# Optimization experiments

Hardware: AMD Instinct MI355X
Metric: run time of the kernel (lower is better)

The kernel has to match this reference:

```python
import jax, jax.numpy as jnp
import numpy as np

B, T, IN, CELL, OUT = 512, 32, 512, 128, 128


def setup_inputs() -> dict:
    key = jax.random.key(0)
    ks = jax.random.split(key, 6)
    d = IN + CELL
    w = lambda k, shape, fan: jax.random.normal(k, shape, jnp.float32) / np.sqrt(fan).astype(np.float32)
    return {
        "x": jax.random.normal(ks[0], (B, T, IN), jnp.float32),
        "Wf": w(ks[1], (d, CELL), d), "bf": jnp.zeros((CELL,), jnp.float32),
        "Wi1": w(ks[2], (d, CELL), d), "bi1": jnp.zeros((CELL,), jnp.float32),
        "Wi2": w(ks[3], (d, CELL), d), "bi2": jnp.zeros((CELL,), jnp.float32),
        "Wo": w(ks[4], (d, CELL), d), "bo": jnp.zeros((CELL,), jnp.float32),
        "Wc": w(ks[5], (CELL, OUT), CELL), "bc": jnp.zeros((OUT,), jnp.float32),
    }


def reference(x, Wf, bf, Wi1, bi1, Wi2, bi2, Wo, bo, Wc, bc):
    # Faithful to MyLSTM.forward: loop runs x.shape[1] times; each iteration
    # concatenates the FULL [B,T,CELL] cell_state with the FULL [B,T,IN] x
    # (x is never sliced per step). Only the last iteration's output matters,
    # but we carry it through the scan to match the loop structure exactly.
    Tn = x.shape[1]
    c0 = jnp.zeros(x.shape[:2] + (Wf.shape[1],), x.dtype)
    out0 = jnp.zeros(x.shape[:2] + (Wc.shape[1],), x.dtype)

    def step(carry, _):
        c, _prev_out = carry
        inp = jnp.concatenate([c, x], axis=-1)  # [B,T,CELL+IN]
        f = jax.nn.sigmoid(inp @ Wf + bf)
        c = c * f + jax.nn.sigmoid(inp @ Wi1 + bi1) * jnp.tanh(inp @ Wi2 + bi2)
        o = jax.nn.sigmoid(inp @ Wo + bo) * jnp.tanh(c)
        out = jax.nn.softmax(o @ Wc + bc, axis=2)  # out_features != 1 branch
        return (c, out), None

    (c, out), _ = jax.lax.scan(step, (c0, out0), None, length=Tn)
    return out, c
```

## Files before the change

### kernel.cpp

```cpp
#include <hip/hip_runtime.h>
#include <stdint.h>

#define ROWS  16384
#define CELL  128
#define INF   512
#define RPB   32
#define NSTEP 32

typedef _Float16 f16x8 __attribute__((ext_vector_type(8)));
typedef _Float16 f16x4 __attribute__((ext_vector_type(4)));
typedef float    f32x16 __attribute__((ext_vector_type(16)));

#define MFMA32(a, b, c) __builtin_amdgcn_mfma_f32_32x32x16_f16((a), (b), (c), 0, 0, 0)

#define AOFF  0
#define XOFF  65536
#define WCOFF 327680
#define WSTOT 344064

__device__ __forceinline__ unsigned short f2h_bits(float f) {
  _Float16 h = (_Float16)f;
  return *(unsigned short*)&h;
}
__device__ __forceinline__ float sig_f(float z) {
  return __builtin_amdgcn_rcpf(1.f + __expf(-z));
}
__device__ __forceinline__ float tanh_f(float z) {
  return 1.f - 2.f * __builtin_amdgcn_rcpf(__expf(2.f * z) + 1.f);
}

__global__ __launch_bounds__(256) void prep_kernel(
    const float* __restrict__ Wf, const float* __restrict__ Wi1,
    const float* __restrict__ Wi2, const float* __restrict__ Wo,
    const float* __restrict__ Wc, unsigned short* __restrict__ ws) {
  int id = blockIdx.x * blockDim.x + threadIdx.x;
  if (id >= WSTOT) return;
  const float* Wg[4] = {Wf, Wi1, Wi2, Wo};
  if (id < XOFF) {
    int g = id >> 14, r = id & 16383;
    int j = r & 7, lane = (r >> 3) & 63, tile = r >> 9;
    int nb = tile & 3, ks = tile >> 2;
    int k = ks * 16 + ((lane >> 5) << 3) + j;
    int n = nb * 32 + (lane & 31);
    ws[id] = f2h_bits(Wg[g][k * CELL + n]);
  } else if (id < WCOFF) {
    int t = id - XOFF;
    int g = t >> 16, r = t & 65535;
    int j = r & 7, lane = (r >> 3) & 63, tile = r >> 9;
    int nb = tile & 3, ks = tile >> 2;
    int k = ks * 16 + ((lane >> 5) << 3) + j;
    int n = nb * 32 + (lane & 31);
    ws[id] = f2h_bits(Wg[g][(CELL + k) * CELL + n]);
  } else {
    int r = id - WCOFF;
    int j = r & 7, lane = (r >> 3) & 63, tile = r >> 9;
    int nb = tile & 3, ks = tile >> 2;
    int k = ks * 16 + ((lane >> 5) << 3) + j;
    int n = nb * 32 + (lane & 31);
    ws[id] = f2h_bits(Wc[k * CELL + n]);
  }
}

__global__ __launch_bounds__(256, 2) void lstm_kernel(
    const float* __restrict__ x,
    const float* __restrict__ bf_, const float* __restrict__ bi1,
    const float* __restrict__ bi2, const float* __restrict__ bo,
    const float* __restrict__ bc,
    const unsigned short* __restrict__ ws, float* __restrict__ out) {

  __shared__ union {
    _Float16 xs[32][264];
    struct {
      _Float16 o[32][136];
      float    s[32][132];
    } ep;
  } uS;
  __shared__ _Float16 cF[2][32][136];
  __shared__ float    uo[32][132];

  const int tid  = threadIdx.x;
  const int lane = tid & 63;
  const int w    = tid >> 6;
  const int n    = lane & 31;
  const int l5   = lane >> 5;
  const int col  = w * 32 + n;
  const int r0   = blockIdx.x * RPB;

  const _Float16* Aw  = (const _Float16*)ws + AOFF;
  const _Float16* Xw  = (const _Float16*)ws + XOFF;
  const _Float16* Wcw = (const _Float16*)ws + WCOFF;

  f32x16 u[4];
#pragma unroll
  for (int g = 0; g < 4; ++g)
#pragma unroll
    for (int i = 0; i < 16; ++i) u[g][i] = 0.f;

  const float* xbase = x + (size_t)r0 * INF;
#pragma unroll 1
  for (int ch = 0; ch < 2; ++ch) {
    if (ch) __syncthreads();
#pragma unroll
    for (int i = 0; i < 8; ++i) {
      int flat = tid + i * 256;
      int row = flat >> 6, c4 = flat & 63;
      const float4 v = ((const float4*)(xbase + (size_t)row * INF + ch * 256))[c4];
      f16x4 h = {(_Float16)v.x, (_Float16)v.y, (_Float16)v.z, (_Float16)v.w};
      *(f16x4*)&uS.xs[row][c4 * 4] = h;
    }
    __syncthreads();
#pragma unroll 2
    for (int ks8 = 0; ks8 < 16; ++ks8) {
      f16x8 a = *(const f16x8*)&uS.xs[n][ks8 * 16 + l5 * 8];
      int ks = ch * 16 + ks8;
#pragma unroll
      for (int g = 0; g < 4; ++g) {
        f16x8 b = *(const f16x8*)(Xw + g * 65536 + ((ks * 4 + w) * 64 + lane) * 8);
        u[g] = MFMA32(a, b, u[g]);
      }
    }
  }
  {
    float b0 = bf_[col], b1 = bi1[col], b2 = bi2[col], b3 = bo[col];
#pragma unroll
    for (int reg = 0; reg < 16; ++reg) {
      u[0][reg] += b0; u[1][reg] += b1; u[2][reg] += b2;
      int r = (reg & 3) + 8 * (reg >> 2) + 4 * l5;
      uo[r][col] = u[3][reg] + b3;
    }
  }

  f16x8 wr[3][8];
#pragma unroll
  for (int g = 0; g < 3; ++g)
#pragma unroll
    for (int ks = 0; ks < 8; ++ks)
      wr[g][ks] = *(const f16x8*)(Aw + g * 16384 + ((ks * 4 + w) * 64 + lane) * 8);

  f32x16 cr;
#pragma unroll
  for (int reg = 0; reg < 16; ++reg) {
    float ig = sig_f(u[1][reg]);
    float gg = tanh_f(u[2][reg]);
    float c0 = ig * gg;
    cr[reg] = c0;
    int r = (reg & 3) + 8 * (reg >> 2) + 4 * l5;
    cF[0][r][col] = (_Float16)c0;
  }
  __syncthreads();

#pragma unroll 1
  for (int t = 1; t < NSTEP - 1; ++t) {
    const int rb = (t + 1) & 1, wb = t & 1;
    f16x8 a[8];
#pragma unroll
    for (int ks = 0; ks < 8; ++ks)
      a[ks] = *(const f16x8*)&cF[rb][n][ks * 16 + l5 * 8];
    f32x16 zf = u[0], zi1 = u[1], zi2 = u[2];
#pragma unroll
    for (int ks = 0; ks < 8; ++ks) {
      zf  = MFMA32(a[ks], wr[0][ks], zf);
      zi1 = MFMA32(a[ks], wr[1][ks], zi1);
      zi2 = MFMA32(a[ks], wr[2][ks], zi2);
    }
#pragma unroll
    for (int reg = 0; reg < 16; ++reg) {
      float fg = sig_f(zf[reg]);
      float ig = sig_f(zi1[reg]);
      float gg = tanh_f(zi2[reg]);
      float cn = fmaf(cr[reg], fg, ig * gg);
      cr[reg] = cn;
      int r = (reg & 3) + 8 * (reg >> 2) + 4 * l5;
      cF[wb][r][col] = (_Float16)cn;
    }
    __syncthreads();
  }

  {
    f16x8 a[8];
#pragma unroll
    for (int ks = 0; ks < 8; ++ks)
      a[ks] = *(const f16x8*)&cF[0][n][ks * 16 + l5 * 8];
    f32x16 zf = u[0], zi1 = u[1], zi2 = u[2], zo;
#pragma unroll
    for (int reg = 0; reg < 16; ++reg) {
      int r = (reg & 3) + 8 * (reg >> 2) + 4 * l5;
      zo[reg] = uo[r][col];
    }
#pragma unroll
    for (int ks = 0; ks < 8; ++ks) {
      f16x8 bo_frag = *(const f16x8*)(Aw + 3 * 16384 + ((ks * 4 + w) * 64 + lane) * 8);
      zf  = MFMA32(a[ks], wr[0][ks], zf);
      zi1 = MFMA32(a[ks], wr[1][ks], zi1);
      zi2 = MFMA32(a[ks], wr[2][ks], zi2);
      zo  = MFMA32(a[ks], bo_frag, zo);
    }
    __syncthreads();
#pragma unroll
    for (int reg = 0; reg < 16; ++reg) {
      float fg = sig_f(zf[reg]);
      float ig = sig_f(zi1[reg]);
      float gg = tanh_f(zi2[reg]);
      float cn = fmaf(cr[reg], fg, ig * gg);
      cr[reg] = cn;
      float ov = sig_f(zo[reg]) * tanh_f(cn);
      int r = (reg & 3) + 8 * (reg >> 2) + 4 * l5;
      uS.ep.o[r][col] = (_Float16)ov;
    }
    __syncthreads();
  }

  {
    f32x16 sacc;
#pragma unroll
    for (int i = 0; i < 16; ++i) sacc[i] = 0.f;
#pragma unroll
    for (int ks = 0; ks < 8; ++ks) {
      f16x8 a = *(const f16x8*)&uS.ep.o[n][ks * 16 + l5 * 8];
      f16x8 b = *(const f16x8*)(Wcw + ((ks * 4 + w) * 64 + lane) * 8);
      sacc = MFMA32(a, b, sacc);
    }
    float bv = bc[col];
#pragma unroll
    for (int reg = 0; reg < 16; ++reg) {
      int r = (reg & 3) + 8 * (reg >> 2) + 4 * l5;
      uS.ep.s[r][col] = sacc[reg] + bv;
    }
    __syncthreads();

#pragma unroll
    for (int rr = 0; rr < 8; ++rr) {
      int r = w * 8 + rr;
      float v0 = uS.ep.s[r][lane];
      float v1 = uS.ep.s[r][lane + 64];
      float m = fmaxf(v0, v1);
#pragma unroll
      for (int off = 32; off; off >>= 1) m = fmaxf(m, __shfl_xor(m, off, 64));
      float e0 = __expf(v0 - m), e1 = __expf(v1 - m);
      float sm = e0 + e1;
#pragma unroll
      for (int off = 32; off; off >>= 1) sm += __shfl_xor(sm, off, 64);
      float inv = __builtin_amdgcn_rcpf(sm);
      size_t base = (size_t)(r0 + r) * 128;
      out[base + lane]      = e0 * inv;
      out[base + lane + 64] = e1 * inv;
    }

#pragma unroll
    for (int reg = 0; reg < 16; ++reg) {
      int r = (reg & 3) + 8 * (reg >> 2) + 4 * l5;
      out[(size_t)ROWS * 128 + (size_t)(r0 + r) * 128 + col] = cr[reg];
    }
  }
}

extern "C" void kernel_launch(void* const* d_in, const int* in_sizes, int n_in,
                              void* d_out, int out_size, void* d_ws, size_t ws_size,
                              hipStream_t stream) {
  const float* x   = (const float*)d_in[0];
  const float* Wf  = (const float*)d_in[1];
  const float* bf_ = (const float*)d_in[2];
  const float* Wi1 = (const float*)d_in[3];
  const float* bi1 = (const float*)d_in[4];
  const float* Wi2 = (const float*)d_in[5];
  const float* bi2 = (const float*)d_in[6];
  const float* Wo  = (const float*)d_in[7];
  const float* bo  = (const float*)d_in[8];
  const float* Wc  = (const float*)d_in[9];
  const float* bc  = (const float*)d_in[10];
  unsigned short* ws = (unsigned short*)d_ws;
  float* out = (float*)d_out;

  hipLaunchKernelGGL(prep_kernel, dim3((WSTOT + 255) / 256), dim3(256), 0, stream,
                     Wf, Wi1, Wi2, Wo, Wc, ws);
  hipLaunchKernelGGL(lstm_kernel, dim3(ROWS / RPB), dim3(256), 0, stream,
                     x, bf_, bi1, bi2, bo, bc, ws, out);
}
```

Before: 179.5 us.

## Switch to 16x16x32 MFMA tiles with 16-row blocks of 512 threads

Each block now handles 16 rows instead of 32 and runs 8 waves of 512 threads, using 16x16x32 MFMA instead of 32x32x16. The prep kernel is reworked to pack the fp16 weights in the new fragment layout. The x chunk is loaded in one pass, and the output-gate preactivation stays in registers instead of shared memory. The aim is to double the grid, raise occupancy and shorten per-step latency on the serial recurrence, at the cost of more blocks repeating weight-register loads and more barriers overall.

```diff
diff --git a/kernel.cpp b/kernel.cpp
--- a/kernel.cpp
+++ b/kernel.cpp
@@ -4,14 +4,14 @@
 #define ROWS  16384
 #define CELL  128
 #define INF   512
-#define RPB   32
+#define RPB   16
 #define NSTEP 32
 
 typedef _Float16 f16x8 __attribute__((ext_vector_type(8)));
 typedef _Float16 f16x4 __attribute__((ext_vector_type(4)));
-typedef float    f32x16 __attribute__((ext_vector_type(16)));
-
-#define MFMA32(a, b, c) __builtin_amdgcn_mfma_f32_32x32x16_f16((a), (b), (c), 0, 0, 0)
+typedef float    f32x4 __attribute__((ext_vector_type(4)));
+
+#define MFMA16(a, b, c) __builtin_amdgcn_mfma_f32_16x16x32_f16((a), (b), (c), 0, 0, 0)
 
 #define AOFF  0
 #define XOFF  65536
@@ -36,201 +36,183 @@
   int id = blockIdx.x * blockDim.x + threadIdx.x;
   if (id >= WSTOT) return;
   const float* Wg[4] = {Wf, Wi1, Wi2, Wo};
+  float v;
+  int k, n, base;
   if (id < XOFF) {
     int g = id >> 14, r = id & 16383;
-    int j = r & 7, lane = (r >> 3) & 63, tile = r >> 9;
-    int nb = tile & 3, ks = tile >> 2;
-    int k = ks * 16 + ((lane >> 5) << 3) + j;
-    int n = nb * 32 + (lane & 31);
-    ws[id] = f2h_bits(Wg[g][k * CELL + n]);
+    k = r >> 7; n = r & 127;
+    v = Wg[g][k * CELL + n];
+    base = g * 16384;
   } else if (id < WCOFF) {
     int t = id - XOFF;
     int g = t >> 16, r = t & 65535;
-    int j = r & 7, lane = (r >> 3) & 63, tile = r >> 9;
-    int nb = tile & 3, ks = tile >> 2;
-    int k = ks * 16 + ((lane >> 5) << 3) + j;
-    int n = nb * 32 + (lane & 31);
-    ws[id] = f2h_bits(Wg[g][(CELL + k) * CELL + n]);
+    k = r >> 7; n = r & 127;
+    v = Wg[g][(CELL + k) * CELL + n];
+    base = XOFF + g * 65536;
   } else {
     int r = id - WCOFF;
-    int j = r & 7, lane = (r >> 3) & 63, tile = r >> 9;
-    int nb = tile & 3, ks = tile >> 2;
-    int k = ks * 16 + ((lane >> 5) << 3) + j;
-    int n = nb * 32 + (lane & 31);
-    ws[id] = f2h_bits(Wc[k * CELL + n]);
-  }
-}
-
-__global__ __launch_bounds__(256, 2) void lstm_kernel(
+    k = r >> 7; n = r & 127;
+    v = Wc[k * CELL + n];
+    base = WCOFF;
+  }
+  int ks = k >> 5, kk = k & 31;
+  int lane = ((kk >> 3) << 4) | (n & 15);
+  int j = kk & 7, nb = n >> 4;
+  ws[base + ((ks * 8 + nb) * 64 + lane) * 8 + j] = f2h_bits(v);
+}
+
+__global__ __launch_bounds__(512, 4) void lstm_kernel(
     const float* __restrict__ x,
     const float* __restrict__ bf_, const float* __restrict__ bi1,
     const float* __restrict__ bi2, const float* __restrict__ bo,
     const float* __restrict__ bc,
     const unsigned short* __restrict__ ws, float* __restrict__ out) {
 
+  __shared__ _Float16 cF[2][16][136];
   __shared__ union {
-    _Float16 xs[32][264];
+    _Float16 xs[16][520];
     struct {
-      _Float16 o[32][136];
-      float    s[32][132];
+      float    s[16][132];
+      _Float16 o[16][136];
     } ep;
   } uS;
-  __shared__ _Float16 cF[2][32][136];
-  __shared__ float    uo[32][132];
 
   const int tid  = threadIdx.x;
   const int lane = tid & 63;
   const int w    = tid >> 6;
-  const int n    = lane & 31;
-  const int l5   = lane >> 5;
-  const int col  = w * 32 + n;
+  const int n16  = lane & 15;
+  const int g4   = lane >> 4;
+  const int col  = w * 16 + n16;
   const int r0   = blockIdx.x * RPB;
 
   const _Float16* Aw  = (const _Float16*)ws + AOFF;
   const _Float16* Xw  = (const _Float16*)ws + XOFF;
   const _Float16* Wcw = (const _Float16*)ws + WCOFF;
 
-  f32x16 u[4];
-#pragma unroll
-  for (int g = 0; g < 4; ++g)
-#pragma unroll
-    for (int i = 0; i < 16; ++i) u[g][i] = 0.f;
-
-  const float* xbase = x + (size_t)r0 * INF;
-#pragma unroll 1
-  for (int ch = 0; ch < 2; ++ch) {
-    if (ch) __syncthreads();
-#pragma unroll
-    for (int i = 0; i < 8; ++i) {
-      int flat = tid + i * 256;
-      int row = flat >> 6, c4 = flat & 63;
-      const float4 v = ((const float4*)(xbase + (size_t)row * INF + ch * 256))[c4];
+  {
+    const float* xb = x + (size_t)r0 * INF;
+#pragma unroll
+    for (int i = 0; i < 4; ++i) {
+      int flat = tid + i * 512;
+      int row = flat >> 7, c4 = flat & 127;
+      const float4 v = ((const float4*)(xb + (size_t)row * INF))[c4];
       f16x4 h = {(_Float16)v.x, (_Float16)v.y, (_Float16)v.z, (_Float16)v.w};
       *(f16x4*)&uS.xs[row][c4 * 4] = h;
     }
-    __syncthreads();
-#pragma unroll 2
-    for (int ks8 = 0; ks8 < 16; ++ks8) {
-      f16x8 a = *(const f16x8*)&uS.xs[n][ks8 * 16 + l5 * 8];
-      int ks = ch * 16 + ks8;
-#pragma unroll
-      for (int g = 0; g < 4; ++g) {
-        f16x8 b = *(const f16x8*)(Xw + g * 65536 + ((ks * 4 + w) * 64 + lane) * 8);
-        u[g] = MFMA32(a, b, u[g]);
-      }
+  }
+  __syncthreads();
+
+  f32x4 u[4];
+#pragma unroll
+  for (int g = 0; g < 4; ++g)
+#pragma unroll
+    for (int i = 0; i < 4; ++i) u[g][i] = 0.f;
+
+#pragma unroll 4
+  for (int ks = 0; ks < 16; ++ks) {
+    f16x8 a = *(const f16x8*)&uS.xs[n16][ks * 32 + g4 * 8];
+#pragma unroll
+    for (int g = 0; g < 4; ++g) {
+      f16x8 b = *(const f16x8*)(Xw + g * 65536 + ((ks * 8 + w) * 64 + lane) * 8);
+      u[g] = MFMA16(a, b, u[g]);
     }
   }
   {
     float b0 = bf_[col], b1 = bi1[col], b2 = bi2[col], b3 = bo[col];
 #pragma unroll
-    for (int reg = 0; reg < 16; ++reg) {
-      u[0][reg] += b0; u[1][reg] += b1; u[2][reg] += b2;
-      int r = (reg & 3) + 8 * (reg >> 2) + 4 * l5;
-      uo[r][col] = u[3][reg] + b3;
-    }
-  }
-
-  f16x8 wr[3][8];
+    for (int i = 0; i < 4; ++i) {
+      u[0][i] += b0; u[1][i] += b1; u[2][i] += b2; u[3][i] += b3;
+    }
+  }
+
+  f16x8 wr[3][4];
 #pragma unroll
   for (int g = 0; g < 3; ++g)
 #pragma unroll
-    for (int ks = 0; ks < 8; ++ks)
-      wr[g][ks] = *(const f16x8*)(Aw + g * 16384 + ((ks * 4 + w) * 64 + lane) * 8);
-
-  f32x16 cr;
-#pragma unroll
-  for (int reg = 0; reg < 16; ++reg) {
-    float ig = sig_f(u[1][reg]);
-    float gg = tanh_f(u[2][reg]);
-    float c0 = ig * gg;
-    cr[reg] = c0;
-    int r = (reg & 3) + 8 * (reg >> 2) + 4 * l5;
-    cF[0][r][col] = (_Float16)c0;
+    for (int ks = 0; ks < 4; ++ks)
+      wr[g][ks] = *(const f16x8*)(Aw + g * 16384 + ((ks * 8 + w) * 64 + lane) * 8);
+
+  f32x4 cr;
+#pragma unroll
+  for (int i = 0; i < 4; ++i) {
+    float c0 = sig_f(u[1][i]) * tanh_f(u[2][i]);
+    cr[i] = c0;
+    cF[0][g4 * 4 + i][col] = (_Float16)c0;
   }
   __syncthreads();
 
 #pragma unroll 1
   for (int t = 1; t < NSTEP - 1; ++t) {
     const int rb = (t + 1) & 1, wb = t & 1;
-    f16x8 a[8];
-#pragma unroll
-    for (int ks = 0; ks < 8; ++ks)
-      a[ks] = *(const f16x8*)&cF[rb][n][ks * 16 + l5 * 8];
-    f32x16 zf = u[0], zi1 = u[1], zi2 = u[2];
-#pragma unroll
-    for (int ks = 0; ks < 8; ++ks) {
-      zf  = MFMA32(a[ks], wr[0][ks], zf);
-      zi1 = MFMA32(a[ks], wr[1][ks], zi1);
-      zi2 = MFMA32(a[ks], wr[2][ks], zi2);
-    }
-#pragma unroll
-    for (int reg = 0; reg < 16; ++reg) {
-      float fg = sig_f(zf[reg]);
-      float ig = sig_f(zi1[reg]);
-      float gg = tanh_f(zi2[reg]);
-      float cn = fmaf(cr[reg], fg, ig * gg);
-      cr[reg] = cn;
-      int r = (reg & 3) + 8 * (reg >> 2) + 4 * l5;
-      cF[wb][r][col] = (_Float16)cn;
+    f16x8 a[4];
+#pragma unroll
+    for (int ks = 0; ks < 4; ++ks)
+      a[ks] = *(const f16x8*)&cF[rb][n16][ks * 32 + g4 * 8];
+    f32x4 zf = u[0], zi1 = u[1], zi2 = u[2];
+#pragma unroll
+    for (int ks = 0; ks < 4; ++ks) {
+      zf  = MFMA16(a[ks], wr[0][ks], zf);
+      zi1 = MFMA16(a[ks], wr[1][ks], zi1);
+      zi2 = MFMA16(a[ks], wr[2][ks], zi2);
+    }
+#pragma unroll
+    for (int i = 0; i < 4; ++i) {
+      float fg = sig_f(zf[i]);
+      float ig = sig_f(zi1[i]);
+      float gg = tanh_f(zi2[i]);
+      float cn = fmaf(cr[i], fg, ig * gg);
+      cr[i] = cn;
+      cF[wb][g4 * 4 + i][col] = (_Float16)cn;
     }
     __syncthreads();
   }
 
   {
-    f16x8 a[8];
-#pragma unroll
-    for (int ks = 0; ks < 8; ++ks)
-      a[ks] = *(const f16x8*)&cF[0][n][ks * 16 + l5 * 8];
-    f32x16 zf = u[0], zi1 = u[1], zi2 = u[2], zo;
-#pragma unroll
-    for (int reg = 0; reg < 16; ++reg) {
-      int r = (reg & 3) + 8 * (reg >> 2) + 4 * l5;
-      zo[reg] = uo[r][col];
-    }
-#pragma unroll
-    for (int ks = 0; ks < 8; ++ks) {
-      f16x8 bo_frag = *(const f16x8*)(Aw + 3 * 16384 + ((ks * 4 + w) * 64 + lane) * 8);
-      zf  = MFMA32(a[ks], wr[0][ks], zf);
-      zi1 = MFMA32(a[ks], wr[1][ks], zi1);
-      zi2 = MFMA32(a[ks], wr[2][ks], zi2);
-      zo  = MFMA32(a[ks], bo_frag, zo);
+    f16x8 a[4];
+#pragma unroll
+    for (int ks = 0; ks < 4; ++ks)
+      a[ks] = *(const f16x8*)&cF[0][n16][ks * 32 + g4 * 8];
+    f32x4 zf = u[0], zi1 = u[1], zi2 = u[2], zo = u[3];
+#pragma unroll
+    for (int ks = 0; ks < 4; ++ks) {
+      f16x8 bo_frag = *(const f16x8*)(Aw + 3 * 16384 + ((ks * 8 + w) * 64 + lane) * 8);
+      zf  = MFMA16(a[ks], wr[0][ks], zf);
+      zi1 = MFMA16(a[ks], wr[1][ks], zi1);
+      zi2 = MFMA16(a[ks], wr[2][ks], zi2);
+      zo  = MFMA16(a[ks], bo_frag, zo);
+    }
+#pragma unroll
+    for (int i = 0; i < 4; ++i) {
+      float fg = sig_f(zf[i]);
+      float ig = sig_f(zi1[i]);
+      float gg = tanh_f(zi2[i]);
+      float cn = fmaf(cr[i], fg, ig * gg);
+      cr[i] = cn;
+      float ov = sig_f(zo[i]) * tanh_f(cn);
+      uS.ep.o[g4 * 4 + i][col] = (_Float16)ov;
     }
     __syncthreads();
-#pragma unroll
-    for (int reg = 0; reg < 16; ++reg) {
-      float fg = sig_f(zf[reg]);
-      float ig = sig_f(zi1[reg]);
-      float gg = tanh_f(zi2[reg]);
-      float cn = fmaf(cr[reg], fg, ig * gg);
-      cr[reg] = cn;
-      float ov = sig_f(zo[reg]) * tanh_f(cn);
-      int r = (reg & 3) + 8 * (reg >> 2) + 4 * l5;
-      uS.ep.o[r][col] = (_Float16)ov;
-    }
+  }
+
+  {
+    f32x4 sacc;
+#pragma unroll
+    for (int i = 0; i < 4; ++i) sacc[i] = 0.f;
+#pragma unroll
+    for (int ks = 0; ks < 4; ++ks) {
+      f16x8 a = *(const f16x8*)&uS.ep.o[n16][ks * 32 + g4 * 8];
+      f16x8 b = *(const f16x8*)(Wcw + ((ks * 8 + w) * 64 + lane) * 8);
+      sacc = MFMA16(a, b, sacc);
+    }
+    float bv = bc[col];
+#pragma unroll
+    for (int i = 0; i < 4; ++i)
+      uS.ep.s[g4 * 4 + i][col] = sacc[i] + bv;
     __syncthreads();
-  }
-
-  {
-    f32x16 sacc;
-#pragma unroll
-    for (int i = 0; i < 16; ++i) sacc[i] = 0.f;
-#pragma unroll
-    for (int ks = 0; ks < 8; ++ks) {
-      f16x8 a = *(const f16x8*)&uS.ep.o[n][ks * 16 + l5 * 8];
-      f16x8 b = *(const f16x8*)(Wcw + ((ks * 4 + w) * 64 + lane) * 8);
-      sacc = MFMA32(a, b, sacc);
-    }
-    float bv = bc[col];
-#pragma unroll
-    for (int reg = 0; reg < 16; ++reg) {
-      int r = (reg & 3) + 8 * (reg >> 2) + 4 * l5;
-      uS.ep.s[r][col] = sacc[reg] + bv;
-    }
-    __syncthreads();
-
-#pragma unroll
-    for (int rr = 0; rr < 8; ++rr) {
-      int r = w * 8 + rr;
+
+#pragma unroll
+    for (int rr = 0; rr < 2; ++rr) {
+      int r = w * 2 + rr;
       float v0 = uS.ep.s[r][lane];
       float v1 = uS.ep.s[r][lane + 64];
       float m = fmaxf(v0, v1);
@@ -247,10 +229,8 @@
     }
 
 #pragma unroll
-    for (int reg = 0; reg < 16; ++reg) {
-      int r = (reg & 3) + 8 * (reg >> 2) + 4 * l5;
-      out[(size_t)ROWS * 128 + (size_t)(r0 + r) * 128 + col] = cr[reg];
-    }
+    for (int i = 0; i < 4; ++i)
+      out[(size_t)ROWS * 128 + (size_t)(r0 + g4 * 4 + i) * 128 + col] = cr[i];
   }
 }
 
@@ -273,6 +253,6 @@
 
   hipLaunchKernelGGL(prep_kernel, dim3((WSTOT + 255) / 256), dim3(256), 0, stream,
                      Wf, Wi1, Wi2, Wo, Wc, ws);
-  hipLaunchKernelGGL(lstm_kernel, dim3(ROWS / RPB), dim3(256), 0, stream,
+  hipLaunchKernelGGL(lstm_kernel, dim3(ROWS / RPB), dim3(512), 0, stream,
                      x, bf_, bi1, bi2, bo, bc, ws, out);
 }
```

After: 170.3 us. 5.1% less time.
